# Optimization experiments

Hardware: AMD Instinct MI355X
Metric: run time of the kernel (lower is better)

The kernel has to match this reference:

```python
import jax, jax.numpy as jnp
import numpy as np

N, E, IN, H, C, ED = 100000, 1600000, 128, 4, 32, 16
HC = H * C
NEG_SLOPE = 0.2
EPS = 1e-5


def setup_inputs() -> dict:
    key = jax.random.key(0)
    ks = jax.random.split(key, 12)
    x = jax.random.normal(ks[0], (N, IN), jnp.float32)
    edge_index = jax.random.randint(ks[1], (2, E), 0, N, dtype=jnp.int32)
    edge_attr = jax.random.normal(ks[2], (E, ED), jnp.float32)
    s_in = 1.0 / np.sqrt(IN)
    s_ed = 1.0 / np.sqrt(ED)
    s_c = 1.0 / np.sqrt(C)
    Wl = jax.random.normal(ks[3], (IN, HC), jnp.float32) * s_in
    bl = jnp.zeros((HC,), jnp.float32)
    Wr = jax.random.normal(ks[4], (IN, HC), jnp.float32) * s_in
    br = jnp.zeros((HC,), jnp.float32)
    We = jax.random.normal(ks[5], (ED, HC), jnp.float32) * s_ed
    att = jax.random.normal(ks[6], (H, C), jnp.float32) * s_c
    bias = jnp.zeros((HC,), jnp.float32)
    ln_weight = jnp.ones((HC,), jnp.float32)
    ln_bias = jnp.zeros((HC,), jnp.float32)
    return {"x": x, "edge_index": edge_index, "edge_attr": edge_attr,
            "Wl": Wl, "bl": bl, "Wr": Wr, "br": br, "We": We,
            "att": att, "bias": bias, "ln_weight": ln_weight, "ln_bias": ln_bias}


def gatv2_block(x, src, dst, edge_attr, Wl, bl, Wr, br, We, att, bias, ln_weight, ln_bias):
    n = x.shape[0]
    xl = (x @ Wl + bl).reshape(n, H, C)  # source-side transform
    xr = (x @ Wr + br).reshape(n, H, C)  # target-side transform
    # add_self_loops with fill_value='mean': self-loop edge_attr = mean of
    # incoming edge_attr per node (0 for isolated nodes)
    ea_sum = jax.ops.segment_sum(edge_attr, dst, num_segments=n)
    cnt = jax.ops.segment_sum(jnp.ones((edge_attr.shape[0],), edge_attr.dtype), dst, num_segments=n)
    self_attr = ea_sum / jnp.maximum(cnt, 1.0)[:, None]
    loop = jnp.arange(n, dtype=src.dtype)
    src_a = jnp.concatenate([src, loop])
    dst_a = jnp.concatenate([dst, loop])
    ea_a = jnp.concatenate([edge_attr, self_attr], axis=0)
    e_emb = (ea_a @ We).reshape(-1, H, C)
    # GATv2 attention: a^T LeakyReLU(xl_j + xr_i + e)
    m = xl[src_a] + xr[dst_a] + e_emb            # [Etot, H, C]
    m = jax.nn.leaky_relu(m, NEG_SLOPE)
    alpha = jnp.einsum('ehc,hc->eh', m, att)     # [Etot, H]
    amax = jax.ops.segment_max(alpha, dst_a, num_segments=n)
    alpha = jnp.exp(alpha - amax[dst_a])
    denom = jax.ops.segment_sum(alpha, dst_a, num_segments=n)
    alpha = alpha / denom[dst_a]
    out = jax.ops.segment_sum(xl[src_a] * alpha[:, :, None], dst_a, num_segments=n)
    h = out.reshape(n, HC) + bias
    # residual (in_dim == H*C so no projection), PyG graph-mode LayerNorm
    z = x + h
    mu = jnp.mean(z)
    var = jnp.mean((z - mu) ** 2)
    z = (z - mu) / jnp.sqrt(var + EPS)
    z = z * ln_weight + ln_bias
    return jax.nn.relu(z)  # dropout = identity in eval


def reference(x, edge_index, edge_attr, Wl, bl, Wr, br, We, att, bias, ln_weight, ln_bias):
    src, dst = edge_index[0], edge_index[1]
    return gatv2_block(x, src, dst, edge_attr, Wl, bl, Wr, br, We, att, bias, ln_weight, ln_bias)
```

## Files before the change

kernel.cpp:

```cpp
#include <hip/hip_runtime.h>
#include <hip/hip_bf16.h>

static constexpr float NEG_SLOPE = 0.2f;
static constexpr float LN_EPS = 1e-5f;

typedef float v2f __attribute__((ext_vector_type(2)));
typedef __attribute__((ext_vector_type(8))) short bf16x8;
typedef __attribute__((ext_vector_type(4))) float f32x4;

__device__ __forceinline__ unsigned f2b(float f) {
  unsigned u = __float_as_uint(f);
  return (u + 0x7fffu + ((u >> 16) & 1u)) >> 16;
}
__device__ __forceinline__ v2f b2f2(ushort2 u) {
  v2f r;
  r.x = __uint_as_float((unsigned)u.x << 16);
  r.y = __uint_as_float((unsigned)u.y << 16);
  return r;
}

__device__ __forceinline__ float head_sum16(float x) {
  float t;
  t = __int_as_float(__builtin_amdgcn_update_dpp(
      0, __float_as_int(x), 0xB1, 0xF, 0xF, true));
  x += t;
  t = __int_as_float(__builtin_amdgcn_update_dpp(
      0, __float_as_int(x), 0x4E, 0xF, 0xF, true));
  x += t;
  t = __int_as_float(__builtin_amdgcn_update_dpp(
      0, __float_as_int(x), 0x124, 0xF, 0xF, true));
  x += t;
  t = __int_as_float(__builtin_amdgcn_update_dpp(
      0, __float_as_int(x), 0x128, 0xF, 0xF, true));
  x += t;
  return x;
}

__global__ __launch_bounds__(256) void k_packB(
    const float* __restrict__ Wl, const float* __restrict__ Wr,
    const float* __restrict__ bl, const float* __restrict__ br,
    ushort* __restrict__ Bpack, float* __restrict__ bcat)
{
  int tid = blockIdx.x * 256 + threadIdx.x;
  int l = tid & 63, s = (tid >> 6) & 3, t = tid >> 8;
  int col = t * 16 + (l & 15);
  int kb = s * 32 + (l >> 4) * 8;
  const float* __restrict__ W = (col < 128) ? Wl : Wr;
  int c = col & 127;
  unsigned p[4];
#pragma unroll
  for (int i = 0; i < 4; ++i) {
    unsigned lo = f2b(W[(size_t)(kb + 2 * i) * 128 + c]);
    unsigned hi = f2b(W[(size_t)(kb + 2 * i + 1) * 128 + c]);
    p[i] = lo | (hi << 16);
  }
  *(uint4*)(Bpack + (size_t)tid * 8) = make_uint4(p[0], p[1], p[2], p[3]);
  if (tid < 256) bcat[tid] = (tid < 128) ? bl[tid] : br[tid - 128];
}

__global__ __launch_bounds__(256) void k_gemm_mfma(
    const float* __restrict__ x, const ushort* __restrict__ Bpack,
    const float* __restrict__ bcat, ushort* __restrict__ xl,
    float* __restrict__ outz, int n)
{
  const int lane = threadIdx.x & 63;
  const int w = threadIdx.x >> 6;
  const int row0 = blockIdx.x * 64 + w * 16;
  const int rowA = min(row0 + (lane & 15), n - 1);
  const int kgrp = lane >> 4;

  f32x4 acc[16];
#pragma unroll
  for (int t = 0; t < 16; ++t) acc[t] = (f32x4){0.f, 0.f, 0.f, 0.f};

#pragma unroll
  for (int s = 0; s < 4; ++s) {
    const float4* ap =
        (const float4*)(x + (size_t)rowA * 128 + s * 32 + kgrp * 8);
    float4 a0 = ap[0], a1 = ap[1];
    bf16x8 a;
    a[0] = (short)f2b(a0.x); a[1] = (short)f2b(a0.y);
    a[2] = (short)f2b(a0.z); a[3] = (short)f2b(a0.w);
    a[4] = (short)f2b(a1.x); a[5] = (short)f2b(a1.y);
    a[6] = (short)f2b(a1.z); a[7] = (short)f2b(a1.w);
#pragma unroll
    for (int t = 0; t < 16; ++t) {
      bf16x8 b =
          *(const bf16x8*)(Bpack + (((size_t)t * 4 + s) * 64 + lane) * 8);
      acc[t] = __builtin_amdgcn_mfma_f32_16x16x32_bf16(a, b, acc[t], 0, 0, 0);
    }
  }

  const int colg = lane & 15;
  const int rbase = row0 + (lane >> 4) * 4;
#pragma unroll
  for (int t = 0; t < 16; ++t) {
    const int col = t * 16 + colg;
    const float bia = bcat[col];
    if (col < 128) {
#pragma unroll
      for (int r = 0; r < 4; ++r) {
        const int R = rbase + r;
        if (R < n) xl[(size_t)R * 128 + col] = (ushort)f2b(acc[t][r] + bia);
      }
    } else {
      const int c = col - 128;
#pragma unroll
      for (int r = 0; r < 4; ++r) {
        const int R = rbase + r;
        if (R < n) outz[(size_t)R * 128 + c] = acc[t][r] + bia;
      }
    }
  }
}

__global__ __launch_bounds__(256) void k_count(const int* __restrict__ dst,
                                               int* __restrict__ deg, int E)
{
  int e = blockIdx.x * 256 + threadIdx.x;
  if (e < E) atomicAdd(&deg[dst[e]], 1);
}

__global__ __launch_bounds__(256) void k_scan1(const int* __restrict__ deg,
                                               int* __restrict__ bsum, int n)
{
  int i = blockIdx.x * 256 + threadIdx.x;
  int v = (i < n) ? deg[i] : 0;
#pragma unroll
  for (int o = 32; o > 0; o >>= 1) v += __shfl_down(v, o);
  __shared__ int ls[4];
  if ((threadIdx.x & 63) == 0) ls[threadIdx.x >> 6] = v;
  __syncthreads();
  if (threadIdx.x == 0) bsum[blockIdx.x] = ls[0] + ls[1] + ls[2] + ls[3];
}

__global__ __launch_bounds__(512) void k_scan2(int* __restrict__ bsum, int nb)
{
  __shared__ int s[512];
  int t = threadIdx.x;
  int v = (t < nb) ? bsum[t] : 0;
  s[t] = v;
  __syncthreads();
  for (int o = 1; o < 512; o <<= 1) {
    int u = (t >= o) ? s[t - o] : 0;
    __syncthreads();
    s[t] += u;
    __syncthreads();
  }
  if (t < nb) bsum[t] = s[t] - v;
}

__global__ __launch_bounds__(256) void k_scan3(const int* __restrict__ deg,
                                               const int* __restrict__ bsum,
                                               int* __restrict__ offs, int n)
{
  __shared__ int s[256];
  int b = blockIdx.x, t = threadIdx.x, i = b * 256 + t;
  int v = (i < n) ? deg[i] : 0;
  s[t] = v;
  __syncthreads();
  for (int o = 1; o < 256; o <<= 1) {
    int u = (t >= o) ? s[t - o] : 0;
    __syncthreads();
    s[t] += u;
    __syncthreads();
  }
  if (i < n) offs[i] = bsum[b] + s[t] - v;
}

__global__ __launch_bounds__(256) void k_fill(
    const int* __restrict__ src, const int* __restrict__ dst,
    const int* __restrict__ offs, int* __restrict__ cursor,
    const float4* __restrict__ ea4, int* __restrict__ csr_src,
    float4* __restrict__ csr_eaf4, int E)
{
  int e = blockIdx.x * 256 + threadIdx.x;
  if (e >= E) return;
  int d = dst[e];
  int pos = offs[d] + atomicAdd(&cursor[d], 1);
  csr_src[pos] = src[e];
  float4 r0 = ea4[(size_t)e * 4 + 0], r1 = ea4[(size_t)e * 4 + 1];
  float4 r2 = ea4[(size_t)e * 4 + 2], r3 = ea4[(size_t)e * 4 + 3];
  float4* o = csr_eaf4 + (size_t)pos * 4;
  o[0] = r0; o[1] = r1; o[2] = r2; o[3] = r3;
}

__global__ __launch_bounds__(256) void k_fused(
    const int* __restrict__ csr_src, const float* __restrict__ eaf,
    const int* __restrict__ offs, const int* __restrict__ deg,
    const ushort* __restrict__ xl, const float* __restrict__ We,
    const float* __restrict__ att, const float* __restrict__ x,
    const float* __restrict__ bias, float* __restrict__ outz,
    double* __restrict__ red, int N)
{
  const int lane = threadIdx.x & 63;
  const int gw =
      __builtin_amdgcn_readfirstlane(blockIdx.x * 4 + (threadIdx.x >> 6));
  const int nw = gridDim.x * 4;
  const v2f* __restrict__ We2 = (const v2f*)We;
  const v2f* __restrict__ X2 = (const v2f*)x;
  v2f* __restrict__ Z2 = (v2f*)outz;

  v2f we[16];
#pragma unroll
  for (int k = 0; k < 16; ++k) we[k] = We2[k * 64 + lane];
  const v2f a2 = ((const v2f*)att)[lane];
  const v2f b2 = ((const v2f*)bias)[lane];
  const bool l16 = lane < 16;

  float sred = 0.f, s2red = 0.f;

  for (int node = gw; node < N; node += nw) {
    const int beg = offs[node];
    const int len = deg[node];
    const v2f xrv = Z2[(size_t)node * 64 + lane];
    const v2f xvSelf =
        b2f2(*(const ushort2*)(xl + (size_t)node * 128 + 2 * lane));

    float mA = -1e30f, dA = 0.f, esA = 0.f;
    float mB = -1e30f, dB = 0.f, esB = 0.f;
    v2f aA = {0.f, 0.f}, aB = {0.f, 0.f};

    auto edgeU = [&](v2f xv, float4 e0, float4 e1, float4 e2, float4 e3,
                     float& m, float& den, v2f& acc) {
      v2f emb = e0.x * we[0];
      emb += e0.y * we[1]; emb += e0.z * we[2]; emb += e0.w * we[3];
      emb += e1.x * we[4]; emb += e1.y * we[5]; emb += e1.z * we[6];
      emb += e1.w * we[7];
      emb += e2.x * we[8]; emb += e2.y * we[9]; emb += e2.z * we[10];
      emb += e2.w * we[11];
      emb += e3.x * we[12]; emb += e3.y * we[13]; emb += e3.z * we[14];
      emb += e3.w * we[15];
      v2f mm = xv + xrv + emb;
      v2f ml;
      ml.x = fmaxf(mm.x, NEG_SLOPE * mm.x);
      ml.y = fmaxf(mm.y, NEG_SLOPE * mm.y);
      const float part = head_sum16(fmaf(ml.y, a2.y, ml.x * a2.x));
      const float mn = fmaxf(m, part);
      const float c = __expf(m - mn);
      const float p = __expf(part - mn);
      den = fmaf(den, c, p);
      acc = acc * c + xv * p;
      m = mn;
    };

    auto selfEdge = [&](v2f xv, float eav, float& m, float& den, v2f& acc) {
      v2f emb = {0.f, 0.f};
#pragma unroll
      for (int k = 0; k < 16; ++k) {
        float eak = __int_as_float(
            __builtin_amdgcn_readlane(__float_as_int(eav), k));
        emb += eak * we[k];
      }
      v2f mm = xv + xrv + emb;
      v2f ml;
      ml.x = fmaxf(mm.x, NEG_SLOPE * mm.x);
      ml.y = fmaxf(mm.y, NEG_SLOPE * mm.y);
      const float part = head_sum16(fmaf(ml.y, a2.y, ml.x * a2.x));
      const float mn = fmaxf(m, part);
      const float c = __expf(m - mn);
      const float p = __expf(part - mn);
      den = fmaf(den, c, p);
      acc = acc * c + xv * p;
      m = mn;
    };

    const int nB = len >> 1;
    const int nA = len - nB;
    const int bB = beg + nA;

    int sA1 = 0, sB1 = 0;
    v2f xvA = {0.f, 0.f}, xvB = {0.f, 0.f};
    if (len > 0) {
      const int sA0 = csr_src[beg];
      xvA = b2f2(*(const ushort2*)(xl + (size_t)sA0 * 128 + 2 * lane));
      sA1 = csr_src[beg + 1];
    }
    if (nB > 0) {
      const int sB0 = csr_src[bB];
      xvB = b2f2(*(const ushort2*)(xl + (size_t)sB0 * 128 + 2 * lane));
      sB1 = csr_src[bB + 1];
    }

    for (int i = 0; i < nB; ++i) {
      const size_t pA = (size_t)(beg + i) * 16;
      const size_t pB = (size_t)(bB + i) * 16;
      const float4* fA = (const float4*)(eaf + pA);
      const float4* fB = (const float4*)(eaf + pB);
      float4 A0 = fA[0], A1 = fA[1], A2 = fA[2], A3 = fA[3];
      float4 B0 = fB[0], B1 = fB[1], B2 = fB[2], B3 = fB[3];
      const float evA = l16 ? eaf[pA + lane] : 0.f;
      const float evB = l16 ? eaf[pB + lane] : 0.f;
      const v2f xvA1 =
          b2f2(*(const ushort2*)(xl + (size_t)sA1 * 128 + 2 * lane));
      const v2f xvB1 =
          b2f2(*(const ushort2*)(xl + (size_t)sB1 * 128 + 2 * lane));
      const int sA2 = csr_src[beg + i + 2];
      const int sB2 = csr_src[bB + i + 2];
      esA += evA;
      esB += evB;
      edgeU(xvA, A0, A1, A2, A3, mA, dA, aA);
      edgeU(xvB, B0, B1, B2, B3, mB, dB, aB);
      xvA = xvA1;
      xvB = xvB1;
      sA1 = sA2;
      sB1 = sB2;
    }
    if (nA > nB) {
      const size_t pA = (size_t)(beg + nA - 1) * 16;
      const float4* fA = (const float4*)(eaf + pA);
      float4 A0 = fA[0], A1 = fA[1], A2 = fA[2], A3 = fA[3];
      const float evA = l16 ? eaf[pA + lane] : 0.f;
      esA += evA;
      edgeU(xvA, A0, A1, A2, A3, mA, dA, aA);
    }
    const float inv = (len > 0) ? 1.f / (float)len : 0.f;
    selfEdge(xvSelf, (esA + esB) * inv, mA, dA, aA);

    const float mn = fmaxf(mA, mB);
    const float cA2 = __expf(mA - mn);
    const float cB2 = __expf(mB - mn);
    const float den = dA * cA2 + dB * cB2;
    const float invden = 1.f / den;
    const float o0 = (aA.x * cA2 + aB.x * cB2) * invden;
    const float o1 = (aA.y * cA2 + aB.y * cB2) * invden;

    const v2f xvn = X2[(size_t)node * 64 + lane];
    const float v0 = xvn.x + o0 + b2.x;
    const float v1 = xvn.y + o1 + b2.y;
    Z2[(size_t)node * 64 + lane] = (v2f){v0, v1};
    sred += v0 + v1;
    s2red += v0 * v0 + v1 * v1;
  }

#pragma unroll
  for (int o = 32; o > 0; o >>= 1) {
    sred += __shfl_down(sred, o);
    s2red += __shfl_down(s2red, o);
  }
  __shared__ double ls[4], ls2[4];
  const int w = threadIdx.x >> 6;
  if ((threadIdx.x & 63) == 0) {
    ls[w] = (double)sred;
    ls2[w] = (double)s2red;
  }
  __syncthreads();
  if (threadIdx.x == 0) {
    unsafeAtomicAdd(red, ls[0] + ls[1] + ls[2] + ls[3]);
    unsafeAtomicAdd(red + 1, ls2[0] + ls2[1] + ls2[2] + ls2[3]);
  }
}

__global__ __launch_bounds__(256) void k_final(
    float* __restrict__ z, const double* __restrict__ red,
    const float* __restrict__ lnw, const float* __restrict__ lnb, int M4)
{
  int i = blockIdx.x * 256 + threadIdx.x;
  if (i >= M4) return;
  const double invM = 1.0 / ((double)M4 * 4.0);
  const double mu = red[0] * invM;
  const double var = red[1] * invM - mu * mu;
  const float sc = rsqrtf((float)var + LN_EPS);
  const float muf = (float)mu;
  const float4* W4 = (const float4*)lnw;
  const float4* L4 = (const float4*)lnb;
  float4* Z4 = (float4*)z;
  float4 zv = Z4[i], wv = W4[i & 31], lv = L4[i & 31];
  float4 o;
  o.x = fmaxf((zv.x - muf) * sc * wv.x + lv.x, 0.f);
  o.y = fmaxf((zv.y - muf) * sc * wv.y + lv.y, 0.f);
  o.z = fmaxf((zv.z - muf) * sc * wv.z + lv.z, 0.f);
  o.w = fmaxf((zv.w - muf) * sc * wv.w + lv.w, 0.f);
  Z4[i] = o;
}

extern "C" void kernel_launch(void* const* d_in, const int* in_sizes, int n_in,
                              void* d_out, int out_size, void* d_ws,
                              size_t ws_size, hipStream_t stream)
{
  const float* x = (const float*)d_in[0];
  const int* ei = (const int*)d_in[1];
  const float* edge_attr = (const float*)d_in[2];
  const float* Wl = (const float*)d_in[3];
  const float* bl = (const float*)d_in[4];
  const float* Wr = (const float*)d_in[5];
  const float* br = (const float*)d_in[6];
  const float* We = (const float*)d_in[7];
  const float* att = (const float*)d_in[8];
  const float* bias = (const float*)d_in[9];
  const float* lnw = (const float*)d_in[10];
  const float* lnb = (const float*)d_in[11];
  float* out = (float*)d_out;

  const int N = in_sizes[0] / 128;
  const int E = in_sizes[1] / 2;
  const int M = N * 128;
  const int* srcp = ei;
  const int* dstp = ei + E;
  const int nb = (N + 255) / 256;

  ushort* xl = (ushort*)d_ws;
  int* deg = (int*)(xl + (size_t)M);
  int* cursor = deg + N;
  int* offs = cursor + N;
  int* bsum = offs + N;
  int* csr_src = bsum + ((nb + 7) & ~7);
  float* csr_eaf =
      (float*)((((size_t)(csr_src + E + 8)) + 63) & ~(size_t)63);
  double* red =
      (double*)((((size_t)(csr_eaf + (size_t)E * 16)) + 15) & ~(size_t)15);
  ushort* Bpack = (ushort*)(red + 2);
  float* bcat = (float*)(Bpack + 4096 * 8);

  hipMemsetAsync(deg, 0, (size_t)N * 8, stream);
  hipMemsetAsync(csr_src + E, 0, 32, stream);
  hipMemsetAsync(red, 0, 16, stream);

  k_packB<<<16, 256, 0, stream>>>(Wl, Wr, bl, br, Bpack, bcat);
  k_gemm_mfma<<<(N + 63) / 64, 256, 0, stream>>>(x, Bpack, bcat, xl, out, N);
  k_count<<<(E + 255) / 256, 256, 0, stream>>>(dstp, deg, E);
  k_scan1<<<nb, 256, 0, stream>>>(deg, bsum, N);
  k_scan2<<<1, 512, 0, stream>>>(bsum, nb);
  k_scan3<<<nb, 256, 0, stream>>>(deg, bsum, offs, N);
  k_fill<<<(E + 255) / 256, 256, 0, stream>>>(srcp, dstp, offs, cursor,
                                              (const float4*)edge_attr,
                                              csr_src, (float4*)csr_eaf, E);
  k_fused<<<2048, 256, 0, stream>>>(csr_src, csr_eaf, offs, deg, xl, We, att,
                                    x, bias, out, red, N);
  k_final<<<(M / 4 + 255) / 256, 256, 0, stream>>>(out, red, lnw, lnb, M / 4);
}
```

Baseline: 568.2 us.

## Store CSR edge attributes as bf16 and prefetch next edge's attributes

The CSR fill kernel now packs edge attributes into bf16 (32 bytes per edge instead of 64), which halves the scattered write traffic in the fill and the streaming read traffic in the fused attention kernel. The fused loop software-pipelines the next edge's attribute load alongside the neighbour feature prefetch, and the fused grid doubles to 4096 blocks. The edge embedding and self-loop mean now use rounded attributes, which adds a small accuracy loss. The prefetch also reads one row past each segment, which relies on padding or the next node's data.

```diff
diff --git a/kernel.cpp b/kernel.cpp
--- a/kernel.cpp
+++ b/kernel.cpp
@@ -17,6 +17,12 @@
   r.x = __uint_as_float((unsigned)u.x << 16);
   r.y = __uint_as_float((unsigned)u.y << 16);
   return r;
+}
+__device__ __forceinline__ float sbl(unsigned w) {
+  return __uint_as_float(w << 16);
+}
+__device__ __forceinline__ float sbh(unsigned w) {
+  return __uint_as_float(w & 0xFFFF0000u);
 }
 
 __device__ __forceinline__ float head_sum16(float x) {
@@ -172,7 +178,7 @@
     const int* __restrict__ src, const int* __restrict__ dst,
     const int* __restrict__ offs, int* __restrict__ cursor,
     const float4* __restrict__ ea4, int* __restrict__ csr_src,
-    float4* __restrict__ csr_eaf4, int E)
+    ushort* __restrict__ csr_ea, int E)
 {
   int e = blockIdx.x * 256 + threadIdx.x;
   if (e >= E) return;
@@ -181,12 +187,15 @@
   csr_src[pos] = src[e];
   float4 r0 = ea4[(size_t)e * 4 + 0], r1 = ea4[(size_t)e * 4 + 1];
   float4 r2 = ea4[(size_t)e * 4 + 2], r3 = ea4[(size_t)e * 4 + 3];
-  float4* o = csr_eaf4 + (size_t)pos * 4;
-  o[0] = r0; o[1] = r1; o[2] = r2; o[3] = r3;
+  uint4* o4 = (uint4*)(csr_ea + (size_t)pos * 16);
+  o4[0] = make_uint4(f2b(r0.x) | (f2b(r0.y) << 16), f2b(r0.z) | (f2b(r0.w) << 16),
+                     f2b(r1.x) | (f2b(r1.y) << 16), f2b(r1.z) | (f2b(r1.w) << 16));
+  o4[1] = make_uint4(f2b(r2.x) | (f2b(r2.y) << 16), f2b(r2.z) | (f2b(r2.w) << 16),
+                     f2b(r3.x) | (f2b(r3.y) << 16), f2b(r3.z) | (f2b(r3.w) << 16));
 }
 
 __global__ __launch_bounds__(256) void k_fused(
-    const int* __restrict__ csr_src, const float* __restrict__ eaf,
+    const int* __restrict__ csr_src, const ushort* __restrict__ csr_ea,
     const int* __restrict__ offs, const int* __restrict__ deg,
     const ushort* __restrict__ xl, const float* __restrict__ We,
     const float* __restrict__ att, const float* __restrict__ x,
@@ -221,16 +230,24 @@
     float mB = -1e30f, dB = 0.f, esB = 0.f;
     v2f aA = {0.f, 0.f}, aB = {0.f, 0.f};
 
-    auto edgeU = [&](v2f xv, float4 e0, float4 e1, float4 e2, float4 e3,
-                     float& m, float& den, v2f& acc) {
-      v2f emb = e0.x * we[0];
-      emb += e0.y * we[1]; emb += e0.z * we[2]; emb += e0.w * we[3];
-      emb += e1.x * we[4]; emb += e1.y * we[5]; emb += e1.z * we[6];
-      emb += e1.w * we[7];
-      emb += e2.x * we[8]; emb += e2.y * we[9]; emb += e2.z * we[10];
-      emb += e2.w * we[11];
-      emb += e3.x * we[12]; emb += e3.y * we[13]; emb += e3.z * we[14];
-      emb += e3.w * we[15];
+    auto edgeU = [&](v2f xv, uint4 lo, uint4 hi, float& m, float& den,
+                     v2f& acc) {
+      v2f emb = sbl(lo.x) * we[0];
+      emb += sbh(lo.x) * we[1];
+      emb += sbl(lo.y) * we[2];
+      emb += sbh(lo.y) * we[3];
+      emb += sbl(lo.z) * we[4];
+      emb += sbh(lo.z) * we[5];
+      emb += sbl(lo.w) * we[6];
+      emb += sbh(lo.w) * we[7];
+      emb += sbl(hi.x) * we[8];
+      emb += sbh(hi.x) * we[9];
+      emb += sbl(hi.y) * we[10];
+      emb += sbh(hi.y) * we[11];
+      emb += sbl(hi.z) * we[12];
+      emb += sbh(hi.z) * we[13];
+      emb += sbl(hi.w) * we[14];
+      emb += sbh(hi.w) * we[15];
       v2f mm = xv + xrv + emb;
       v2f ml;
       ml.x = fmaxf(mm.x, NEG_SLOPE * mm.x);
@@ -269,28 +286,46 @@
     const int nA = len - nB;
     const int bB = beg + nA;
 
+    uint4 eAlo = {0, 0, 0, 0}, eAhi = {0, 0, 0, 0};
+    uint4 eBlo = {0, 0, 0, 0}, eBhi = {0, 0, 0, 0};
+    float evA = 0.f, evB = 0.f;
+    v2f xvA = {0.f, 0.f}, xvB = {0.f, 0.f};
     int sA1 = 0, sB1 = 0;
-    v2f xvA = {0.f, 0.f}, xvB = {0.f, 0.f};
+
     if (len > 0) {
+      const uint4* pa = (const uint4*)(csr_ea + (size_t)beg * 16);
+      eAlo = pa[0];
+      eAhi = pa[1];
+      evA = l16 ? __uint_as_float((unsigned)csr_ea[(size_t)beg * 16 + lane]
+                                  << 16)
+                : 0.f;
       const int sA0 = csr_src[beg];
       xvA = b2f2(*(const ushort2*)(xl + (size_t)sA0 * 128 + 2 * lane));
       sA1 = csr_src[beg + 1];
     }
     if (nB > 0) {
+      const uint4* pb = (const uint4*)(csr_ea + (size_t)bB * 16);
+      eBlo = pb[0];
+      eBhi = pb[1];
+      evB = l16 ? __uint_as_float((unsigned)csr_ea[(size_t)bB * 16 + lane]
+                                  << 16)
+                : 0.f;
       const int sB0 = csr_src[bB];
       xvB = b2f2(*(const ushort2*)(xl + (size_t)sB0 * 128 + 2 * lane));
       sB1 = csr_src[bB + 1];
     }
 
     for (int i = 0; i < nB; ++i) {
-      const size_t pA = (size_t)(beg + i) * 16;
-      const size_t pB = (size_t)(bB + i) * 16;
-      const float4* fA = (const float4*)(eaf + pA);
-      const float4* fB = (const float4*)(eaf + pB);
-      float4 A0 = fA[0], A1 = fA[1], A2 = fA[2], A3 = fA[3];
-      float4 B0 = fB[0], B1 = fB[1], B2 = fB[2], B3 = fB[3];
-      const float evA = l16 ? eaf[pA + lane] : 0.f;
-      const float evB = l16 ? eaf[pB + lane] : 0.f;
+      const size_t qA = (size_t)(beg + i + 1) * 16;
+      const size_t qB = (size_t)(bB + i + 1) * 16;
+      const uint4* pa = (const uint4*)(csr_ea + qA);
+      const uint4* pb = (const uint4*)(csr_ea + qB);
+      const uint4 nAlo = pa[0], nAhi = pa[1];
+      const uint4 nBlo = pb[0], nBhi = pb[1];
+      const float evA1 =
+          l16 ? __uint_as_float((unsigned)csr_ea[qA + lane] << 16) : 0.f;
+      const float evB1 =
+          l16 ? __uint_as_float((unsigned)csr_ea[qB + lane] << 16) : 0.f;
       const v2f xvA1 =
           b2f2(*(const ushort2*)(xl + (size_t)sA1 * 128 + 2 * lane));
       const v2f xvB1 =
@@ -299,20 +334,16 @@
       const int sB2 = csr_src[bB + i + 2];
       esA += evA;
       esB += evB;
-      edgeU(xvA, A0, A1, A2, A3, mA, dA, aA);
-      edgeU(xvB, B0, B1, B2, B3, mB, dB, aB);
-      xvA = xvA1;
-      xvB = xvB1;
-      sA1 = sA2;
-      sB1 = sB2;
+      edgeU(xvA, eAlo, eAhi, mA, dA, aA);
+      edgeU(xvB, eBlo, eBhi, mB, dB, aB);
+      eAlo = nAlo; eAhi = nAhi; eBlo = nBlo; eBhi = nBhi;
+      evA = evA1; evB = evB1;
+      xvA = xvA1; xvB = xvB1;
+      sA1 = sA2; sB1 = sB2;
     }
     if (nA > nB) {
-      const size_t pA = (size_t)(beg + nA - 1) * 16;
-      const float4* fA = (const float4*)(eaf + pA);
-      float4 A0 = fA[0], A1 = fA[1], A2 = fA[2], A3 = fA[3];
-      const float evA = l16 ? eaf[pA + lane] : 0.f;
       esA += evA;
-      edgeU(xvA, A0, A1, A2, A3, mA, dA, aA);
+      edgeU(xvA, eAlo, eAhi, mA, dA, aA);
     }
     const float inv = (len > 0) ? 1.f / (float)len : 0.f;
     selfEdge(xvSelf, (esA + esB) * inv, mA, dA, aA);
@@ -405,11 +436,11 @@
   int* offs = cursor + N;
   int* bsum = offs + N;
   int* csr_src = bsum + ((nb + 7) & ~7);
-  float* csr_eaf =
-      (float*)((((size_t)(csr_src + E + 8)) + 63) & ~(size_t)63);
+  ushort* csr_ea =
+      (ushort*)((((size_t)(csr_src + E + 8)) + 63) & ~(size_t)63);
   double* red =
-      (double*)((((size_t)(csr_eaf + (size_t)E * 16)) + 15) & ~(size_t)15);
-  ushort* Bpack = (ushort*)(red + 2);
+      (double*)((((size_t)(csr_ea + (size_t)E * 16)) + 127) & ~(size_t)127);
+  ushort* Bpack = (ushort*)(red + 8);
   float* bcat = (float*)(Bpack + 4096 * 8);
 
   hipMemsetAsync(deg, 0, (size_t)N * 8, stream);
@@ -424,8 +455,8 @@
   k_scan3<<<nb, 256, 0, stream>>>(deg, bsum, offs, N);
   k_fill<<<(E + 255) / 256, 256, 0, stream>>>(srcp, dstp, offs, cursor,
                                               (const float4*)edge_attr,
-                                              csr_src, (float4*)csr_eaf, E);
-  k_fused<<<2048, 256, 0, stream>>>(csr_src, csr_eaf, offs, deg, xl, We, att,
+                                              csr_src, csr_ea, E);
+  k_fused<<<4096, 256, 0, stream>>>(csr_src, csr_ea, offs, deg, xl, We, att,
                                     x, bias, out, red, N);
   k_final<<<(M / 4 + 255) / 256, 256, 0, stream>>>(out, red, lnw, lnb, M / 4);
 }
```

Measured after the change: 566.0 us. No clear change (-0.4%).
